# Kernel optimization log

Measured on AMD Instinct MI355X. Metric: run time of the kernel, lower is better.

Reference implementation:

```python
import jax, jax.numpy as jnp
import numpy as np

P = 8    # patch_size
N = 16   # n_patches
WS = 32  # window_size


def setup_inputs() -> dict:
    key = jax.random.key(0)
    k1, k2 = jax.random.split(key)
    B, C, H, W = 8, 12, 512, 512
    return {
        "data_real": jax.random.normal(k1, (B, C, H, W), dtype=jnp.float32),
        "data_imag": jax.random.normal(k2, (B, C, H, W), dtype=jnp.float32),
        "ref_x": 248,
        "ref_y": 248,
    }


def reference(data_real, data_imag, ref_x, ref_y):
    p, n, ws = P, N, WS
    # complex64 represented as trailing real/imag axis (matches torch.view_as_real)
    data = jnp.stack([data_real, data_imag], axis=-1)  # [B,C,H,W,2]
    B, C, H, W, _ = data.shape

    # reference patch at (ref_x, ref_y)
    ref = data[:, :, ref_x:ref_x + p, ref_y:ref_y + p, :]  # [B,C,p,p,2]

    # clamped search window (static Python ints -> static shapes)
    wx0 = max(ref_x - ws // 2, 0); wx1 = min(ref_x + ws // 2, H)
    wy0 = max(ref_y - ws // 2, 0); wy1 = min(ref_y + ws // 2, W)
    win = data[:, :, wx0:wx1, wy0:wy1, :]  # [B,C,Wh,Ww,2]
    Wh, Ww = win.shape[2], win.shape[3]
    Ph, Pw = Wh - p + 1, Ww - p + 1

    # all sliding patches in the window, vectorized via fancy indexing
    ix = jnp.arange(Ph)[:, None] + jnp.arange(p)[None, :]  # [Ph,p]
    iy = jnp.arange(Pw)[:, None] + jnp.arange(p)[None, :]  # [Pw,p]
    patches = win[:, :, ix[:, None, :, None], iy[None, :, None, :], :]  # [B,C,Ph,Pw,p,p,2]

    # mse_loss over view_as_real == 0.5 * mean(|diff|^2) over p*p complex elems
    diff = patches - ref[:, :, None, None]
    dists = 0.5 * jnp.mean(diff * diff, axis=(-3, -2, -1))  # [B,C,Ph,Pw]

    M = Ph * Pw  # row-major (x outer, y inner) matches the torch loop order
    dists = dists.reshape(B, C, M)
    pats = patches.reshape(B, C, M, p * p, 2)

    slot = jnp.arange(n)

    def select(dv, pv):  # dv: [M], pv: [M, p*p, 2]
        def step(carry, inp):
            nd, ns = carry
            di, pi = inp
            mask = nd > di                      # candidate slots
            oh = (slot == jnp.argmax(mask)) & jnp.any(mask)  # first True slot
            nd = jnp.where(oh, di, nd)
            ns = jnp.where(oh[:, None, None], pi, ns)
            return (nd, ns), None

        init = (jnp.full((n,), 1e33, dtype=dv.dtype),
                jnp.zeros((n, p * p, 2), dtype=pv.dtype))
        (nd, ns), _ = jax.lax.scan(step, init, (dv, pv))
        return ns

    # independent sequential top-n insertion per (batch, contrast)
    sims = jax.vmap(jax.vmap(select))(dists, pats)  # [B,C,n,p*p,2]
    return sims
```

## Files before the change

### kernel.cpp

```cpp
#include <hip/hip_runtime.h>
#include <math.h>

#define PP    8
#define NSEL  16
#define WSZ   32

__global__ __launch_bounds__(256) void patches_select_kernel(
    const float* __restrict__ d_re,
    const float* __restrict__ d_im,
    const int*   __restrict__ p_rx,
    const int*   __restrict__ p_ry,
    float*       __restrict__ out,
    int H, int W)
{
    const int bc  = blockIdx.x;
    const int tid = threadIdx.x;

    const int rx = p_rx[0];
    const int ry = p_ry[0];
    const int wx0 = max(rx - WSZ / 2, 0);
    const int wx1 = min(rx + WSZ / 2, H);
    const int wy0 = max(ry - WSZ / 2, 0);
    const int wy1 = min(ry + WSZ / 2, W);
    const int Wh = wx1 - wx0;
    const int Ww = wy1 - wy0;
    const int Ph = Wh - PP + 1;
    const int Pw = Ww - PP + 1;
    const int M  = Ph * Pw;
    const int Mpad = (M + 15) & ~15;

    __shared__ float sre[WSZ][WSZ];
    __shared__ float sim[WSZ][WSZ];
    __shared__ float sref[PP][PP][2];
    __shared__ float dists[WSZ * WSZ];
    __shared__ int   selIdx[NSEL];

    const size_t plane = (size_t)H * W;
    const float* baseR = d_re + (size_t)bc * plane;
    const float* baseI = d_im + (size_t)bc * plane;

    for (int t = tid; t < Wh * Ww; t += 256) {
        const int i = t / Ww, j = t - i * Ww;
        const size_t g = (size_t)(wx0 + i) * W + (wy0 + j);
        sre[i][j] = baseR[g];
        sim[i][j] = baseI[g];
    }
    for (int t = tid; t < PP * PP; t += 256) {
        const int i = t / PP, j = t - i * PP;
        const size_t g = (size_t)(rx + i) * W + (ry + j);
        sref[i][j][0] = baseR[g];
        sref[i][j][1] = baseI[g];
    }
    if (tid < 16 && M + tid < Mpad) dists[M + tid] = INFINITY;
    __syncthreads();

    for (int m = tid; m < M; m += 256) {
        const int pi = m / Pw, pj = m - pi * Pw;
        float r[8];
#pragma unroll
        for (int j = 0; j < 8; ++j) r[j] = 0.0f;
#pragma unroll
        for (int k = 0; k < 16; ++k) {
            const int dx  = k >> 1;
            const int dyb = (k & 1) * 4;
#pragma unroll
            for (int j = 0; j < 8; ++j) {
                const int dy   = dyb + (j >> 1);
                const int comp = j & 1;
                const float w  = comp ? sim[pi + dx][pj + dy] : sre[pi + dx][pj + dy];
                const float rf = sref[dx][dy][comp];
                const float dl = __fsub_rn(w, rf);
                const float sq = __fmul_rn(dl, dl);
                r[j] = __fadd_rn(r[j], sq);
            }
        }
        const float s0 = __fadd_rn(__fadd_rn(r[0], r[1]), __fadd_rn(r[2], r[3]));
        const float s1 = __fadd_rn(__fadd_rn(r[4], r[5]), __fadd_rn(r[6], r[7]));
        const float S  = __fadd_rn(s0, s1);
        dists[m] = S * (1.0f / 256.0f);
    }
    __syncthreads();

    if (tid < 64) {
        float nd  = (tid < NSEL) ? 1e33f : -1.0f;
        int   mi  = -1;
        float cur[16];
#pragma unroll
        for (int u = 0; u < 16; ++u) cur[u] = dists[u];
        for (int m0 = 0; m0 < Mpad; m0 += 16) {
            float nxt[16];
            const int nb = m0 + 16;
            if (nb < Mpad) {
#pragma unroll
                for (int u = 0; u < 16; ++u) nxt[u] = dists[nb + u];
            } else {
#pragma unroll
                for (int u = 0; u < 16; ++u) nxt[u] = INFINITY;
            }
#pragma unroll
            for (int u = 0; u < 16; ++u) {
                const unsigned long long mask = __ballot(nd > cur[u]);
                const int first = __ffsll(mask) - 1;
                if (tid == first) { nd = cur[u]; mi = m0 + u; }
            }
#pragma unroll
            for (int u = 0; u < 16; ++u) cur[u] = nxt[u];
        }
        if (tid < NSEL) selIdx[tid] = mi;
    }
    __syncthreads();

    float* obase = out + (size_t)bc * (NSEL * PP * PP * 2);
    for (int t = tid; t < NSEL * PP * PP * 2; t += 256) {
        const int slot = t >> 7;
        const int rem  = t & 127;
        const int k    = rem >> 1;
        const int comp = rem & 1;
        const int m    = selIdx[slot];
        float v = 0.0f;
        if (m >= 0) {
            const int pi = m / Pw, pj = m - pi * Pw;
            const int dx = k >> 3, dy = k & 7;
            v = comp ? sim[pi + dx][pj + dy] : sre[pi + dx][pj + dy];
        }
        obase[t] = v;
    }
}

extern "C" void kernel_launch(void* const* d_in, const int* in_sizes, int n_in,
                              void* d_out, int out_size, void* d_ws, size_t ws_size,
                              hipStream_t stream) {
    const float* d_re = (const float*)d_in[0];
    const float* d_im = (const float*)d_in[1];
    const int*   p_rx = (const int*)d_in[2];
    const int*   p_ry = (const int*)d_in[3];
    float* out = (float*)d_out;

    const int H = 512, W = 512;
    const int BC = in_sizes[0] / (H * W);

    patches_select_kernel<<<BC, 256, 0, stream>>>(d_re, d_im, p_rx, p_ry, out, H, W);
}
```

Before: 196.7 us.

## Vectorize window loads, batch distance rows, run selection in every wave

The window is now loaded with float4 global loads when it is aligned and unclamped, and reference values are read as float4 from shared memory. Each thread's candidate positions are processed together inside the k loop, reusing each reference read. All four waves run the ballot-based top-16 insertion redundantly, so selected indices reach output threads by wave shuffle instead of through shared memory and an extra barrier. Output is written as two float4 stores per thread. The cost is redundant selection work in every wave and higher register pressure from the acc[3][8] arrays.

```diff
diff --git a/kernel.cpp b/kernel.cpp
--- a/kernel.cpp
+++ b/kernel.cpp
@@ -13,8 +13,9 @@
     float*       __restrict__ out,
     int H, int W)
 {
-    const int bc  = blockIdx.x;
-    const int tid = threadIdx.x;
+    const int bc   = blockIdx.x;
+    const int tid  = threadIdx.x;
+    const int lane = tid & 63;
 
     const int rx = p_rx[0];
     const int ry = p_ry[0];
@@ -29,61 +30,89 @@
     const int M  = Ph * Pw;
     const int Mpad = (M + 15) & ~15;
 
-    __shared__ float sre[WSZ][WSZ];
-    __shared__ float sim[WSZ][WSZ];
-    __shared__ float sref[PP][PP][2];
+    __shared__ __align__(16) float sre[WSZ][WSZ];
+    __shared__ __align__(16) float sim_[WSZ][WSZ];
+    __shared__ __align__(16) float sref[PP * PP * 2];
     __shared__ float dists[WSZ * WSZ];
-    __shared__ int   selIdx[NSEL];
 
     const size_t plane = (size_t)H * W;
     const float* baseR = d_re + (size_t)bc * plane;
     const float* baseI = d_im + (size_t)bc * plane;
 
-    for (int t = tid; t < Wh * Ww; t += 256) {
-        const int i = t / Ww, j = t - i * Ww;
-        const size_t g = (size_t)(wx0 + i) * W + (wy0 + j);
-        sre[i][j] = baseR[g];
-        sim[i][j] = baseI[g];
+    if (Wh == WSZ && Ww == WSZ && ((wy0 & 3) == 0) && ((W & 3) == 0)) {
+        const int nv = WSZ * (WSZ / 4);
+        for (int t = tid; t < nv; t += 256) {
+            const int i = t >> 3, j4 = (t & 7) << 2;
+            const size_t g = (size_t)(wx0 + i) * W + (wy0 + j4);
+            *(float4*)&sre[i][j4]  = *(const float4*)&baseR[g];
+            *(float4*)&sim_[i][j4] = *(const float4*)&baseI[g];
+        }
+    } else {
+        for (int t = tid; t < Wh * Ww; t += 256) {
+            const int i = t / Ww, j = t - i * Ww;
+            const size_t g = (size_t)(wx0 + i) * W + (wy0 + j);
+            sre[i][j]  = baseR[g];
+            sim_[i][j] = baseI[g];
+        }
     }
     for (int t = tid; t < PP * PP; t += 256) {
         const int i = t / PP, j = t - i * PP;
         const size_t g = (size_t)(rx + i) * W + (ry + j);
-        sref[i][j][0] = baseR[g];
-        sref[i][j][1] = baseI[g];
+        sref[t * 2 + 0] = baseR[g];
+        sref[t * 2 + 1] = baseI[g];
     }
     if (tid < 16 && M + tid < Mpad) dists[M + tid] = INFINITY;
     __syncthreads();
 
-    for (int m = tid; m < M; m += 256) {
-        const int pi = m / Pw, pj = m - pi * Pw;
-        float r[8];
+    {
+        int nm = 0;
+        int mlist[3], mpi[3], mpj[3];
+        for (int m = tid; m < M; m += 256) {
+            mlist[nm] = m; mpi[nm] = m / Pw; mpj[nm] = m - (m / Pw) * Pw; ++nm;
+        }
+        float acc[3][8];
 #pragma unroll
-        for (int j = 0; j < 8; ++j) r[j] = 0.0f;
+        for (int mm = 0; mm < 3; ++mm)
+#pragma unroll
+            for (int j = 0; j < 8; ++j) acc[mm][j] = 0.0f;
+
+        const float4* ref4 = (const float4*)sref;
 #pragma unroll
         for (int k = 0; k < 16; ++k) {
+            const float4 ra = ref4[2 * k];
+            const float4 rb = ref4[2 * k + 1];
             const int dx  = k >> 1;
             const int dyb = (k & 1) * 4;
-#pragma unroll
-            for (int j = 0; j < 8; ++j) {
-                const int dy   = dyb + (j >> 1);
-                const int comp = j & 1;
-                const float w  = comp ? sim[pi + dx][pj + dy] : sre[pi + dx][pj + dy];
-                const float rf = sref[dx][dy][comp];
-                const float dl = __fsub_rn(w, rf);
-                const float sq = __fmul_rn(dl, dl);
-                r[j] = __fadd_rn(r[j], sq);
+            for (int mm = 0; mm < nm; ++mm) {
+                const float* wr = &sre[mpi[mm] + dx][mpj[mm] + dyb];
+                const float* wi = &sim_[mpi[mm] + dx][mpj[mm] + dyb];
+                const float w0 = wr[0], w1 = wr[1], w2 = wr[2], w3 = wr[3];
+                const float v0 = wi[0], v1 = wi[1], v2 = wi[2], v3 = wi[3];
+                float d;
+                d = __fsub_rn(w0, ra.x); acc[mm][0] = __fadd_rn(acc[mm][0], __fmul_rn(d, d));
+                d = __fsub_rn(v0, ra.y); acc[mm][1] = __fadd_rn(acc[mm][1], __fmul_rn(d, d));
+                d = __fsub_rn(w1, ra.z); acc[mm][2] = __fadd_rn(acc[mm][2], __fmul_rn(d, d));
+                d = __fsub_rn(v1, ra.w); acc[mm][3] = __fadd_rn(acc[mm][3], __fmul_rn(d, d));
+                d = __fsub_rn(w2, rb.x); acc[mm][4] = __fadd_rn(acc[mm][4], __fmul_rn(d, d));
+                d = __fsub_rn(v2, rb.y); acc[mm][5] = __fadd_rn(acc[mm][5], __fmul_rn(d, d));
+                d = __fsub_rn(w3, rb.z); acc[mm][6] = __fadd_rn(acc[mm][6], __fmul_rn(d, d));
+                d = __fsub_rn(v3, rb.w); acc[mm][7] = __fadd_rn(acc[mm][7], __fmul_rn(d, d));
             }
         }
-        const float s0 = __fadd_rn(__fadd_rn(r[0], r[1]), __fadd_rn(r[2], r[3]));
-        const float s1 = __fadd_rn(__fadd_rn(r[4], r[5]), __fadd_rn(r[6], r[7]));
-        const float S  = __fadd_rn(s0, s1);
-        dists[m] = S * (1.0f / 256.0f);
+        for (int mm = 0; mm < nm; ++mm) {
+            const float s0 = __fadd_rn(__fadd_rn(acc[mm][0], acc[mm][1]),
+                                       __fadd_rn(acc[mm][2], acc[mm][3]));
+            const float s1 = __fadd_rn(__fadd_rn(acc[mm][4], acc[mm][5]),
+                                       __fadd_rn(acc[mm][6], acc[mm][7]));
+            const float S  = __fadd_rn(s0, s1);
+            dists[mlist[mm]] = S * (1.0f / 256.0f);
+        }
     }
     __syncthreads();
 
-    if (tid < 64) {
-        float nd  = (tid < NSEL) ? 1e33f : -1.0f;
-        int   mi  = -1;
+    float nd = (lane < NSEL) ? 1e33f : -1.0f;
+    int   mi = -1;
+    {
         float cur[16];
 #pragma unroll
         for (int u = 0; u < 16; ++u) cur[u] = dists[u];
@@ -101,30 +130,33 @@
             for (int u = 0; u < 16; ++u) {
                 const unsigned long long mask = __ballot(nd > cur[u]);
                 const int first = __ffsll(mask) - 1;
-                if (tid == first) { nd = cur[u]; mi = m0 + u; }
+                if (lane == first) { nd = cur[u]; mi = m0 + u; }
             }
 #pragma unroll
             for (int u = 0; u < 16; ++u) cur[u] = nxt[u];
         }
-        if (tid < NSEL) selIdx[tid] = mi;
     }
-    __syncthreads();
 
-    float* obase = out + (size_t)bc * (NSEL * PP * PP * 2);
-    for (int t = tid; t < NSEL * PP * PP * 2; t += 256) {
-        const int slot = t >> 7;
-        const int rem  = t & 127;
-        const int k    = rem >> 1;
-        const int comp = rem & 1;
-        const int m    = selIdx[slot];
-        float v = 0.0f;
-        if (m >= 0) {
-            const int pi = m / Pw, pj = m - pi * Pw;
-            const int dx = k >> 3, dy = k & 7;
-            v = comp ? sim[pi + dx][pj + dy] : sre[pi + dx][pj + dy];
+    const int slot = tid >> 4;
+    const int m = __shfl(mi, slot);
+    float* obase = out + (size_t)bc * (NSEL * PP * PP * 2) + tid * 8;
+    const int rem0 = (tid & 15) * 8;
+    float vals[8];
+    if (m >= 0) {
+        const int pi = m / Pw, pj = m - (m / Pw) * Pw;
+#pragma unroll
+        for (int q = 0; q < 8; ++q) {
+            const int e = rem0 + q;
+            const int kk = e >> 1, comp = e & 1;
+            const int dx = kk >> 3, dy = kk & 7;
+            vals[q] = comp ? sim_[pi + dx][pj + dy] : sre[pi + dx][pj + dy];
         }
-        obase[t] = v;
+    } else {
+#pragma unroll
+        for (int q = 0; q < 8; ++q) vals[q] = 0.0f;
     }
+    *(float4*)&obase[0] = make_float4(vals[0], vals[1], vals[2], vals[3]);
+    *(float4*)&obase[4] = make_float4(vals[4], vals[5], vals[6], vals[7]);
 }
 
 extern "C" void kernel_launch(void* const* d_in, const int* in_sizes, int n_in,
```

New measurement: 242.3 us. 1.23x slower.
